# Optimization experiments

Hardware: AMD Instinct MI355X
Metric: run time of the kernel (lower is better)

## Reference

```python
import jax, jax.numpy as jnp
import numpy as np

N_ATOMS = 262144
BATCH = 4096
HIDDEN = 256
HEADS = 4
SCALE = (HIDDEN // HEADS) ** -0.5
LN_EPS = 1e-5
SM_EPS = 1e-16


def setup_inputs() -> dict:
    key = jax.random.key(0)
    ks = jax.random.split(key, 10)
    s = HIDDEN ** -0.5
    return {
        "drug_atoms": jax.random.normal(ks[0], (N_ATOMS, HIDDEN), jnp.float32),
        "protein_ctx": jax.random.normal(ks[1], (BATCH, HIDDEN), jnp.float32),
        "batch_index": jnp.sort(jax.random.randint(ks[2], (N_ATOMS,), 0, BATCH)),
        "Wq": jax.random.normal(ks[3], (HIDDEN, HIDDEN), jnp.float32) * s,
        "bq": jnp.zeros((HIDDEN,), jnp.float32),
        "Wk": jax.random.normal(ks[4], (HIDDEN, HIDDEN), jnp.float32) * s,
        "bk": jnp.zeros((HIDDEN,), jnp.float32),
        "Wv": jax.random.normal(ks[5], (HIDDEN, HIDDEN), jnp.float32) * s,
        "bv": jnp.zeros((HIDDEN,), jnp.float32),
        "ln_gamma": jnp.ones((HIDDEN,), jnp.float32),
        "ln_beta": jnp.zeros((HIDDEN,), jnp.float32),
    }


def _segment_softmax(logits, seg, num_segments):
    # logits: [N, 1]; segment-wise stable softmax (torch_geometric.utils.softmax)
    m = jax.ops.segment_max(logits, seg, num_segments=num_segments)  # [B, 1]
    e = jnp.exp(logits - m[seg])
    s = jax.ops.segment_sum(e, seg, num_segments=num_segments)  # [B, 1]
    return e / (s[seg] + SM_EPS)


def _layer_norm(x, gamma, beta):
    mu = jnp.mean(x, axis=-1, keepdims=True)
    var = jnp.mean(jnp.square(x - mu), axis=-1, keepdims=True)
    return (x - mu) * jax.lax.rsqrt(var + LN_EPS) * gamma + beta


def reference(drug_atoms, protein_ctx, batch_index, Wq, bq, Wk, bk, Wv, bv, ln_gamma, ln_beta):
    protein_expanded = protein_ctx[batch_index]  # [N, H] gather
    Q = protein_expanded @ Wq + bq
    K = drug_atoms @ Wk + bk
    V = drug_atoms @ Wv + bv
    dots = jnp.sum(Q * K, axis=-1, keepdims=True) * SCALE  # [N, 1]
    attn = _segment_softmax(dots, batch_index, BATCH)  # [N, 1]
    out = attn * V + drug_atoms  # weighted V + residual
    return _layer_norm(out, ln_gamma, ln_beta), attn
```

## Files before the change

### kernel.cpp

```cpp
#include <hip/hip_runtime.h>
#include <hip/hip_bf16.h>

#define N_ATOMS 262144
#define BATCH   4096
#define HID     256

typedef __attribute__((ext_vector_type(8))) short short8;
typedef __attribute__((ext_vector_type(4))) float f32x4;
typedef unsigned short u16;
typedef unsigned int   u32;

__device__ __forceinline__ float bf2f(u16 h){
    u32 x = ((u32)h) << 16;
    return __builtin_bit_cast(float, x);
}
__device__ __forceinline__ u16 f2bf(float f){
    u32 x = __builtin_bit_cast(u32, f);
    u32 r = (x + 0x7FFFu + ((x >> 16) & 1u)) >> 16;
    return (u16)r;
}
__device__ __forceinline__ int probe_isf32(const u32* p){
    return ((p[0] & 0xFFFFu) == 0u) ? 1 : 0;
}
__device__ __forceinline__ float cvt_any(const void* p, size_t i, int isf32){
    return isf32 ? ((const float*)p)[i] : bf2f(((const u16*)p)[i]);
}

__global__ void prep_kernel(const void* Wq, const void* Wk, const void* Wv,
                            const void* bq, const void* bk, const void* bv,
                            const void* gamma, const void* beta,
                            float* __restrict__ WqF, float* __restrict__ WkTF,
                            u16* __restrict__ Wfrag,
                            u32* __restrict__ menc, float* __restrict__ sbuf,
                            float* __restrict__ bqf, float* __restrict__ bkf,
                            float* __restrict__ bvf, float* __restrict__ gamf,
                            float* __restrict__ betf){
    const int isf32 = probe_isf32((const u32*)gamma);
    int blk = blockIdx.x, t = threadIdx.x;
    if (blk < 256){
        size_t i = (size_t)blk*HID + t;
        WqF[i] = cvt_any(Wq, i, isf32);
    } else if (blk < 512){
        int k = blk - 256;
        WkTF[(size_t)k*HID + t] = cvt_any(Wk, (size_t)t*HID + k, isf32);
    } else if (blk < 768){
        int n = blk - 512;
        int k = t;
        int ntile = n >> 4, l15 = n & 15;
        int ki = k >> 5, quad = (k >> 3) & 3, e = k & 7;
        int off = ((ntile*8 + ki)*4 + quad)*128 + l15*8 + e;
        Wfrag[off] = f2bf(cvt_any(Wv, (size_t)k*HID + n, isf32));
    } else if (blk < 784){
        int i = (blk - 768)*256 + t;
        menc[i] = 0u; sbuf[i] = 0.f;
    } else {
        bqf[t]  = cvt_any(bq, t, isf32);
        bkf[t]  = cvt_any(bk, t, isf32);
        bvf[t]  = cvt_any(bv, t, isf32);
        gamf[t] = cvt_any(gamma, t, isf32);
        betf[t] = cvt_any(beta, t, isf32);
    }
}

template<int AMODE, int BIAS>
__global__ void small_gemm(const void* Araw, const float* __restrict__ BknF,
                           const float* __restrict__ biasF,
                           float* __restrict__ outF, const u32* __restrict__ probe){
    __shared__ float As[8*HID];
    const int t  = threadIdx.x;
    const int rb = blockIdx.x * 8;
    const int isf32 = AMODE ? 1 : probe_isf32(probe);
    #pragma unroll
    for (int i = 0; i < 8; ++i)
        As[i*HID + t] = cvt_any(Araw, (size_t)(rb + i)*HID + t, isf32);
    __syncthreads();
    float acc[8] = {0.f,0.f,0.f,0.f,0.f,0.f,0.f,0.f};
    for (int j = 0; j < HID; j += 4){
        float w0 = BknF[(size_t)(j+0)*HID + t];
        float w1 = BknF[(size_t)(j+1)*HID + t];
        float w2 = BknF[(size_t)(j+2)*HID + t];
        float w3 = BknF[(size_t)(j+3)*HID + t];
        #pragma unroll
        for (int r = 0; r < 8; ++r){
            float4 a = *(const float4*)(As + r*HID + j);
            acc[r] += a.x*w0 + a.y*w1 + a.z*w2 + a.w*w3;
        }
    }
    float b = BIAS ? biasF[t] : 0.f;
    #pragma unroll
    for (int r = 0; r < 8; ++r)
        outF[(size_t)(rb + r)*HID + t] = acc[r] + b;
}

__global__ void ck_kernel(const float* __restrict__ Qf, const float* __restrict__ bkf,
                          float* __restrict__ cvec){
    int row  = blockIdx.x*4 + (threadIdx.x >> 6);
    int lane = threadIdx.x & 63;
    float4 q = *(const float4*)(Qf + (size_t)row*HID + lane*4);
    float p = q.x*bkf[lane*4] + q.y*bkf[lane*4+1] + q.z*bkf[lane*4+2] + q.w*bkf[lane*4+3];
    #pragma unroll
    for (int off=1; off<64; off<<=1) p += __shfl_xor(p, off, 64);
    if (lane == 0) cvec[row] = p;
}

__global__ void dots_kernel(const void* xraw, const int* __restrict__ bidx,
                            const float* __restrict__ uF, const float* __restrict__ cvec,
                            float* __restrict__ dots, u32* __restrict__ menc,
                            const u32* __restrict__ probe){
    const int isf32 = probe_isf32(probe);
    int row  = blockIdx.x*4 + (threadIdx.x >> 6);
    int lane = threadIdx.x & 63;
    int b = bidx[row];
    float4 uv = *(const float4*)(uF + (size_t)b*HID + lane*4);
    float p;
    if (isf32){
        float4 xv = *(const float4*)((const float*)xraw + (size_t)row*HID + lane*4);
        p = xv.x*uv.x + xv.y*uv.y + xv.z*uv.z + xv.w*uv.w;
    } else {
        ushort4 xv = *(const ushort4*)((const u16*)xraw + (size_t)row*HID + lane*4);
        p = bf2f(xv.x)*uv.x + bf2f(xv.y)*uv.y + bf2f(xv.z)*uv.z + bf2f(xv.w)*uv.w;
    }
    #pragma unroll
    for (int off=1; off<64; off<<=1) p += __shfl_xor(p, off, 64);
    if (lane == 0){
        float d = (p + cvec[b]) * 0.125f;
        if (!(fabsf(d) < 1e30f)) d = 0.f;
        dots[row] = d;
        u32 bits = __builtin_bit_cast(u32, d);
        u32 key = (bits & 0x80000000u) ? ~bits : (bits | 0x80000000u);
        atomicMax(&menc[b], key);
    }
}

__global__ void expsum_kernel(const int* __restrict__ bidx, const u32* __restrict__ menc,
                              float* __restrict__ dots, float* __restrict__ sbuf){
    int n    = blockIdx.x*256 + threadIdx.x;
    int lane = threadIdx.x & 63;
    int b = bidx[n];
    u32 key = menc[b];
    u32 bits = (key & 0x80000000u) ? (key & 0x7FFFFFFFu) : ~key;
    float m = __builtin_bit_cast(float, bits);
    float ev = __expf(dots[n] - m);
    dots[n] = ev;
    int b0  = __shfl(b, 0, 64);
    int b63 = __shfl(b, 63, 64);
    if (b0 == b63){
        float t = ev;
        #pragma unroll
        for (int off=1; off<64; off<<=1) t += __shfl_xor(t, off, 64);
        if (lane == 0) atomicAdd(&sbuf[b], t);
    } else {
        atomicAdd(&sbuf[b], ev);
    }
}

__launch_bounds__(256, 4)
__global__ void main_fused(const void* xraw, const u16* __restrict__ Wfrag,
                           const float* __restrict__ ebuf, const float* __restrict__ sbuf,
                           const int* __restrict__ bidx,
                           const float* __restrict__ bvf, const float* __restrict__ gamf,
                           const float* __restrict__ betf,
                           void* outraw, const u32* __restrict__ probe)
{
    __shared__ u16 Abuf[64*HID];
    __shared__ float attn_lds[64];
    __shared__ float bv_lds[HID];
    __shared__ float rowsum[64];
    __shared__ float rowsq[64];

    const int tid  = threadIdx.x;
    const int lane = tid & 63;
    const int wave = tid >> 6;
    const int quad = lane >> 4;
    const int l15  = lane & 15;
    const int rowBase = blockIdx.x * 64;
    const int isf32 = probe_isf32(probe);

    if (isf32){
        const float* Af = (const float*)xraw;
        #pragma unroll
        for (int iss = 0; iss < 8; ++iss){
            int g = iss*256 + tid; int r = g>>5, c = g&31;
            const float* p = Af + (size_t)(rowBase + r)*HID + c*8;
            float4 f0 = *(const float4*)p;
            float4 f1 = *(const float4*)(p + 4);
            short8 s;
            s[0]=(short)f2bf(f0.x); s[1]=(short)f2bf(f0.y);
            s[2]=(short)f2bf(f0.z); s[3]=(short)f2bf(f0.w);
            s[4]=(short)f2bf(f1.x); s[5]=(short)f2bf(f1.y);
            s[6]=(short)f2bf(f1.z); s[7]=(short)f2bf(f1.w);
            int cp = c ^ (r & 7);
            *(short8*)(Abuf + r*256 + cp*8) = s;
        }
    } else {
        const u16* Ab = (const u16*)xraw;
        short8 areg[8];
        #pragma unroll
        for (int iss = 0; iss < 8; ++iss){
            int g = iss*256 + tid; int r = g>>5, c = g&31;
            areg[iss] = *(const short8*)(Ab + (size_t)(rowBase + r)*HID + c*8);
        }
        #pragma unroll
        for (int iss = 0; iss < 8; ++iss){
            int g = iss*256 + tid; int r = g>>5, c = g&31;
            int cp = c ^ (r & 7);
            *(short8*)(Abuf + r*256 + cp*8) = areg[iss];
        }
    }

    if (tid < 64){
        int rowG = rowBase + tid;
        int b = bidx[rowG];
        float at = ebuf[rowG] / (sbuf[b] + 1e-16f);
        if (!(fabsf(at) < 1e30f)) at = 0.f;
        attn_lds[tid] = at;
        if (isf32) (((float*)outraw) + (size_t)N_ATOMS*HID)[rowG] = at;
        else       (((u16*)outraw)  + (size_t)N_ATOMS*HID)[rowG] = f2bf(at);
        rowsum[tid] = 0.f;
        rowsq[tid]  = 0.f;
    }
    bv_lds[tid] = bvf[tid];

    float gam[4], bet[4];
    #pragma unroll
    for (int ct = 0; ct < 4; ++ct){
        int col = wave*64 + ct*16 + l15;
        gam[ct] = gamf[col];
        bet[ct] = betf[col];
    }

    f32x4 acc[4][4];
    #pragma unroll
    for (int rt=0; rt<4; ++rt)
      #pragma unroll
      for (int ct=0; ct<4; ++ct)
        acc[rt][ct] = (f32x4){0.f,0.f,0.f,0.f};

    __syncthreads();

    for (int ki = 0; ki < 8; ++ki){
        short8 bfr[4];
        #pragma unroll
        for (int ct=0; ct<4; ++ct){
            int ntile = wave*4 + ct;
            bfr[ct] = *(const short8*)(Wfrag + (size_t)((ntile*8 + ki)*512) + lane*8);
        }
        short8 af[4];
        #pragma unroll
        for (int rt=0; rt<4; ++rt){
            int r  = rt*16 + l15;
            int cc = ki*4 + quad;
            int cp = cc ^ (r & 7);
            af[rt] = *(const short8*)(Abuf + r*256 + cp*8);
        }
        #pragma unroll
        for (int rt=0; rt<4; ++rt)
          #pragma unroll
          for (int ct=0; ct<4; ++ct)
            acc[rt][ct] = __builtin_amdgcn_mfma_f32_16x16x32_bf16(
                              af[rt], bfr[ct], acc[rt][ct], 0, 0, 0);
    }

    #pragma unroll
    for (int rt=0; rt<4; ++rt)
      #pragma unroll
      for (int ct=0; ct<4; ++ct)
        #pragma unroll
        for (int i=0; i<4; ++i){
            int row = rt*16 + quad*4 + i;
            int col = wave*64 + ct*16 + l15;
            int cc = col >> 3;
            int cp = cc ^ (row & 7);
            float xv = bf2f(Abuf[row*256 + cp*8 + (col & 7)]);
            acc[rt][ct][i] = attn_lds[row] * (acc[rt][ct][i] + bv_lds[col]) + xv;
        }
    #pragma unroll
    for (int rt=0; rt<4; ++rt)
      #pragma unroll
      for (int i=0; i<4; ++i){
          float s1 = 0.f, s2 = 0.f;
          #pragma unroll
          for (int ct=0; ct<4; ++ct){ float v = acc[rt][ct][i]; s1 += v; s2 += v*v; }
          #pragma unroll
          for (int off=1; off<16; off<<=1){
              s1 += __shfl_xor(s1, off, 64);
              s2 += __shfl_xor(s2, off, 64);
          }
          if (l15 == 0){
              int row = rt*16 + quad*4 + i;
              atomicAdd(&rowsum[row], s1);
              atomicAdd(&rowsq[row],  s2);
          }
      }
    __syncthreads();
    #pragma unroll
    for (int rt=0; rt<4; ++rt)
      #pragma unroll
      for (int i=0; i<4; ++i){
          int row = rt*16 + quad*4 + i;
          float mu  = rowsum[row] * (1.f/256.f);
          float var = fmaxf(rowsq[row] * (1.f/256.f) - mu*mu, 0.f);
          float rstd = rsqrtf(var + 1e-5f);
          #pragma unroll
          for (int ct=0; ct<4; ++ct){
              int col = wave*64 + ct*16 + l15;
              float v = (acc[rt][ct][i] - mu) * rstd * gam[ct] + bet[ct];
              size_t idx = (size_t)(rowBase+row)*HID + col;
              if (isf32) ((float*)outraw)[idx] = v;
              else       ((u16*)outraw)[idx]  = f2bf(v);
          }
      }
}

extern "C" void kernel_launch(void* const* d_in, const int* in_sizes, int n_in,
                              void* d_out, int out_size, void* d_ws, size_t ws_size,
                              hipStream_t stream) {
    const void* x    = d_in[0];
    const void* P    = d_in[1];
    const int*  bidx = (const int*)d_in[2];
    const void* Wq   = d_in[3];
    const void* bq   = d_in[4];
    const void* Wk   = d_in[5];
    const void* bk   = d_in[6];
    const void* Wv   = d_in[7];
    const void* bv   = d_in[8];
    const void* gam  = d_in[9];
    const void* bet  = d_in[10];
    const u32* probe = (const u32*)gam;

    char* ws = (char*)d_ws;
    float* WqF  = (float*)(ws);
    float* WkTF = (float*)(ws + 262144);
    u16*   Wfrag= (u16*)  (ws + 524288);
    float* Qf   = (float*)(ws + 655360);
    float* uF   = (float*)(ws + 4849664);
    float* cvec = (float*)(ws + 9043968);
    u32*   menc = (u32*)  (ws + 9060352);
    float* sbuf = (float*)(ws + 9076736);
    float* dots = (float*)(ws + 9093120);
    float* bqf  = (float*)(ws + 10141696);
    float* bkf  = (float*)(ws + 10142720);
    float* bvf  = (float*)(ws + 10143744);
    float* gamf = (float*)(ws + 10144768);
    float* betf = (float*)(ws + 10145792);

    prep_kernel<<<785, 256, 0, stream>>>(Wq, Wk, Wv, bq, bk, bv, gam, bet,
                                         WqF, WkTF, Wfrag, menc, sbuf,
                                         bqf, bkf, bvf, gamf, betf);
    small_gemm<0,1><<<BATCH/8, 256, 0, stream>>>(P, WqF, bqf, Qf, probe);
    small_gemm<1,0><<<BATCH/8, 256, 0, stream>>>(Qf, WkTF, nullptr, uF, probe);
    ck_kernel<<<BATCH/4, 256, 0, stream>>>(Qf, bkf, cvec);
    dots_kernel<<<N_ATOMS/4, 256, 0, stream>>>(x, bidx, uF, cvec, dots, menc, probe);
    expsum_kernel<<<N_ATOMS/256, 256, 0, stream>>>(bidx, menc, dots, sbuf);
    main_fused<<<N_ATOMS/64, 256, 0, stream>>>(x, Wfrag, dots, sbuf, bidx,
                                               bvf, gamf, betf, d_out, probe);
}
```

Baseline: 820.1 us.

## Precompute Wq·WkT, drop segment max, stage output stores through LDS

The Q/K projection is refactored algebraically. M = Wq·Wk^T and the bias terms are precomputed, so the per-batch u vector comes from a single small GEMM on protein_ctx. The segment-max pass and the expsum kernel are removed: exponentials are computed directly in dots_kernel after clamping logits to ±80, with per-block combined atomic sums. The main kernel's LayerNorm output is transposed through LDS so it can be written with coalesced vector nontemporal stores. Skipping the max subtraction changes numerical behaviour, risking overflow or precision loss for large logits, though the clamp bounds it.

```diff
diff --git a/kernel.cpp b/kernel.cpp
--- a/kernel.cpp
+++ b/kernel.cpp
@@ -7,6 +7,7 @@
 
 typedef __attribute__((ext_vector_type(8))) short short8;
 typedef __attribute__((ext_vector_type(4))) float f32x4;
+typedef __attribute__((ext_vector_type(4))) unsigned short u16x4;
 typedef unsigned short u16;
 typedef unsigned int   u32;
 
@@ -26,33 +27,29 @@
     return isf32 ? ((const float*)p)[i] : bf2f(((const u16*)p)[i]);
 }
 
-__global__ void prep_kernel(const void* Wq, const void* Wk, const void* Wv,
+__global__ void prep_kernel(const void* Wk, const void* Wv,
                             const void* bq, const void* bk, const void* bv,
                             const void* gamma, const void* beta,
-                            float* __restrict__ WqF, float* __restrict__ WkTF,
-                            u16* __restrict__ Wfrag,
-                            u32* __restrict__ menc, float* __restrict__ sbuf,
+                            float* __restrict__ WkTF, u16* __restrict__ Wfrag,
+                            float* __restrict__ sbuf,
                             float* __restrict__ bqf, float* __restrict__ bkf,
                             float* __restrict__ bvf, float* __restrict__ gamf,
                             float* __restrict__ betf){
     const int isf32 = probe_isf32((const u32*)gamma);
     int blk = blockIdx.x, t = threadIdx.x;
     if (blk < 256){
-        size_t i = (size_t)blk*HID + t;
-        WqF[i] = cvt_any(Wq, i, isf32);
+        int k = blk;
+        WkTF[(size_t)k*HID + t] = cvt_any(Wk, (size_t)t*HID + k, isf32);
     } else if (blk < 512){
-        int k = blk - 256;
-        WkTF[(size_t)k*HID + t] = cvt_any(Wk, (size_t)t*HID + k, isf32);
-    } else if (blk < 768){
-        int n = blk - 512;
+        int n = blk - 256;
         int k = t;
         int ntile = n >> 4, l15 = n & 15;
         int ki = k >> 5, quad = (k >> 3) & 3, e = k & 7;
         int off = ((ntile*8 + ki)*4 + quad)*128 + l15*8 + e;
         Wfrag[off] = f2bf(cvt_any(Wv, (size_t)k*HID + n, isf32));
-    } else if (blk < 784){
-        int i = (blk - 768)*256 + t;
-        menc[i] = 0u; sbuf[i] = 0.f;
+    } else if (blk < 528){
+        int i = (blk - 512)*256 + t;
+        sbuf[i] = 0.f;
     } else {
         bqf[t]  = cvt_any(bq, t, isf32);
         bkf[t]  = cvt_any(bk, t, isf32);
@@ -92,23 +89,53 @@
         outF[(size_t)(rb + r)*HID + t] = acc[r] + b;
 }
 
-__global__ void ck_kernel(const float* __restrict__ Qf, const float* __restrict__ bkf,
-                          float* __restrict__ cvec){
+__global__ void vb_kernel(const float* __restrict__ WkTF,
+                          const float* __restrict__ bqf, const float* __restrict__ bkf,
+                          float* __restrict__ v0F, float* __restrict__ s0){
+    __shared__ float ws4[4];
+    int t = threadIdx.x;
+    float a = 0.f;
+    for (int j = 0; j < HID; ++j)
+        a += bqf[j] * WkTF[(size_t)j*HID + t];
+    v0F[t] = a;
+    float p = bqf[t]*bkf[t];
+    #pragma unroll
+    for (int off=1; off<64; off<<=1) p += __shfl_xor(p, off, 64);
+    if ((t & 63) == 0) ws4[t >> 6] = p;
+    __syncthreads();
+    if (t == 0) s0[0] = ws4[0]+ws4[1]+ws4[2]+ws4[3];
+}
+
+template<int ADDS>
+__global__ void rowdot_kernel(const void* Araw, const float* __restrict__ vecF,
+                              const float* __restrict__ s0, float* __restrict__ outv,
+                              const u32* __restrict__ probe){
+    const int isf32 = probe_isf32(probe);
     int row  = blockIdx.x*4 + (threadIdx.x >> 6);
     int lane = threadIdx.x & 63;
-    float4 q = *(const float4*)(Qf + (size_t)row*HID + lane*4);
-    float p = q.x*bkf[lane*4] + q.y*bkf[lane*4+1] + q.z*bkf[lane*4+2] + q.w*bkf[lane*4+3];
+    float4 vv = *(const float4*)(vecF + lane*4);
+    float p;
+    if (isf32){
+        float4 av = *(const float4*)((const float*)Araw + (size_t)row*HID + lane*4);
+        p = av.x*vv.x + av.y*vv.y + av.z*vv.z + av.w*vv.w;
+    } else {
+        ushort4 av = *(const ushort4*)((const u16*)Araw + (size_t)row*HID + lane*4);
+        p = bf2f(av.x)*vv.x + bf2f(av.y)*vv.y + bf2f(av.z)*vv.z + bf2f(av.w)*vv.w;
+    }
     #pragma unroll
     for (int off=1; off<64; off<<=1) p += __shfl_xor(p, off, 64);
-    if (lane == 0) cvec[row] = p;
+    if (lane == 0) outv[row] = p + (ADDS ? s0[0] : 0.f);
 }
 
 __global__ void dots_kernel(const void* xraw, const int* __restrict__ bidx,
                             const float* __restrict__ uF, const float* __restrict__ cvec,
-                            float* __restrict__ dots, u32* __restrict__ menc,
+                            float* __restrict__ ebuf, float* __restrict__ sbuf,
                             const u32* __restrict__ probe){
+    __shared__ float eS[4];
+    __shared__ int   bS[4];
     const int isf32 = probe_isf32(probe);
     int row  = blockIdx.x*4 + (threadIdx.x >> 6);
+    int wave = threadIdx.x >> 6;
     int lane = threadIdx.x & 63;
     int b = bidx[row];
     float4 uv = *(const float4*)(uF + (size_t)b*HID + lane*4);
@@ -122,35 +149,23 @@
     }
     #pragma unroll
     for (int off=1; off<64; off<<=1) p += __shfl_xor(p, off, 64);
+    float ev = 0.f;
     if (lane == 0){
         float d = (p + cvec[b]) * 0.125f;
-        if (!(fabsf(d) < 1e30f)) d = 0.f;
-        dots[row] = d;
-        u32 bits = __builtin_bit_cast(u32, d);
-        u32 key = (bits & 0x80000000u) ? ~bits : (bits | 0x80000000u);
-        atomicMax(&menc[b], key);
-    }
-}
-
-__global__ void expsum_kernel(const int* __restrict__ bidx, const u32* __restrict__ menc,
-                              float* __restrict__ dots, float* __restrict__ sbuf){
-    int n    = blockIdx.x*256 + threadIdx.x;
-    int lane = threadIdx.x & 63;
-    int b = bidx[n];
-    u32 key = menc[b];
-    u32 bits = (key & 0x80000000u) ? (key & 0x7FFFFFFFu) : ~key;
-    float m = __builtin_bit_cast(float, bits);
-    float ev = __expf(dots[n] - m);
-    dots[n] = ev;
-    int b0  = __shfl(b, 0, 64);
-    int b63 = __shfl(b, 63, 64);
-    if (b0 == b63){
-        float t = ev;
-        #pragma unroll
-        for (int off=1; off<64; off<<=1) t += __shfl_xor(t, off, 64);
-        if (lane == 0) atomicAdd(&sbuf[b], t);
-    } else {
-        atomicAdd(&sbuf[b], ev);
+        if (!(fabsf(d) < 80.f)) d = (d > 0.f) ? 80.f : -80.f;
+        ev = __expf(d);
+        ebuf[row] = ev;
+        eS[wave] = ev; bS[wave] = b;
+    }
+    __syncthreads();
+    if (threadIdx.x == 0){
+        float a = eS[0]; int cb = bS[0];
+        #pragma unroll
+        for (int w = 1; w < 4; ++w){
+            if (bS[w] == cb) a += eS[w];
+            else { atomicAdd(&sbuf[cb], a); cb = bS[w]; a = eS[w]; }
+        }
+        atomicAdd(&sbuf[cb], a);
     }
 }
 
@@ -293,6 +308,7 @@
           }
       }
     __syncthreads();
+
     #pragma unroll
     for (int rt=0; rt<4; ++rt)
       #pragma unroll
@@ -302,14 +318,49 @@
           float var = fmaxf(rowsq[row] * (1.f/256.f) - mu*mu, 0.f);
           float rstd = rsqrtf(var + 1e-5f);
           #pragma unroll
-          for (int ct=0; ct<4; ++ct){
-              int col = wave*64 + ct*16 + l15;
-              float v = (acc[rt][ct][i] - mu) * rstd * gam[ct] + bet[ct];
-              size_t idx = (size_t)(rowBase+row)*HID + col;
-              if (isf32) ((float*)outraw)[idx] = v;
-              else       ((u16*)outraw)[idx]  = f2bf(v);
-          }
+          for (int ct=0; ct<4; ++ct)
+              acc[rt][ct][i] = (acc[rt][ct][i] - mu) * rstd * gam[ct] + bet[ct];
       }
+
+    float* AbufF = (float*)Abuf;
+    #pragma unroll
+    for (int h = 0; h < 2; ++h){
+        if (h) __syncthreads();
+        #pragma unroll
+        for (int rtl = 0; rtl < 2; ++rtl){
+            int rt = 2*h + rtl;
+            #pragma unroll
+            for (int ct=0; ct<4; ++ct)
+              #pragma unroll
+              for (int i=0; i<4; ++i){
+                  int rl  = rtl*16 + quad*4 + i;
+                  int col = wave*64 + ct*16 + l15;
+                  AbufF[rl*256 + col] = acc[rt][ct][i];
+              }
+        }
+        __syncthreads();
+        size_t obase = (size_t)rowBase*HID + (size_t)h*8192;
+        if (isf32){
+            f32x4* og = (f32x4*)((float*)outraw + obase);
+            #pragma unroll
+            for (int s = 0; s < 8; ++s){
+                int f4 = s*256 + tid;
+                f32x4 v4 = ((const f32x4*)AbufF)[f4];
+                __builtin_nontemporal_store(v4, og + f4);
+            }
+        } else {
+            u16x4* og = (u16x4*)((u16*)outraw + obase);
+            #pragma unroll
+            for (int s = 0; s < 8; ++s){
+                int f4 = s*256 + tid;
+                f32x4 v4 = ((const f32x4*)AbufF)[f4];
+                u16x4 u;
+                u.x = f2bf(v4.x); u.y = f2bf(v4.y);
+                u.z = f2bf(v4.z); u.w = f2bf(v4.w);
+                __builtin_nontemporal_store(u, og + f4);
+            }
+        }
+    }
 }
 
 extern "C" void kernel_launch(void* const* d_in, const int* in_sizes, int n_in,
@@ -329,29 +380,31 @@
     const u32* probe = (const u32*)gam;
 
     char* ws = (char*)d_ws;
-    float* WqF  = (float*)(ws);
-    float* WkTF = (float*)(ws + 262144);
-    u16*   Wfrag= (u16*)  (ws + 524288);
-    float* Qf   = (float*)(ws + 655360);
-    float* uF   = (float*)(ws + 4849664);
-    float* cvec = (float*)(ws + 9043968);
-    u32*   menc = (u32*)  (ws + 9060352);
-    float* sbuf = (float*)(ws + 9076736);
-    float* dots = (float*)(ws + 9093120);
-    float* bqf  = (float*)(ws + 10141696);
-    float* bkf  = (float*)(ws + 10142720);
-    float* bvf  = (float*)(ws + 10143744);
-    float* gamf = (float*)(ws + 10144768);
-    float* betf = (float*)(ws + 10145792);
-
-    prep_kernel<<<785, 256, 0, stream>>>(Wq, Wk, Wv, bq, bk, bv, gam, bet,
-                                         WqF, WkTF, Wfrag, menc, sbuf,
+    float* WkTF = (float*)(ws);
+    u16*   Wfrag= (u16*)  (ws + 262144);
+    float* M    = (float*)(ws + 393216);
+    float* uF   = (float*)(ws + 655360);
+    float* cvec = (float*)(ws + 4849664);
+    float* sbuf = (float*)(ws + 4866048);
+    float* ebuf = (float*)(ws + 4882432);
+    float* bqf  = (float*)(ws + 5931008);
+    float* bkf  = (float*)(ws + 5932032);
+    float* bvf  = (float*)(ws + 5933056);
+    float* gamf = (float*)(ws + 5934080);
+    float* betf = (float*)(ws + 5935104);
+    float* v0F  = (float*)(ws + 5936128);
+    float* w1f  = (float*)(ws + 5937152);
+    float* s0b  = (float*)(ws + 5938176);
+
+    prep_kernel<<<529, 256, 0, stream>>>(Wk, Wv, bq, bk, bv, gam, bet,
+                                         WkTF, Wfrag, sbuf,
                                          bqf, bkf, bvf, gamf, betf);
-    small_gemm<0,1><<<BATCH/8, 256, 0, stream>>>(P, WqF, bqf, Qf, probe);
-    small_gemm<1,0><<<BATCH/8, 256, 0, stream>>>(Qf, WkTF, nullptr, uF, probe);
-    ck_kernel<<<BATCH/4, 256, 0, stream>>>(Qf, bkf, cvec);
-    dots_kernel<<<N_ATOMS/4, 256, 0, stream>>>(x, bidx, uF, cvec, dots, menc, probe);
-    expsum_kernel<<<N_ATOMS/256, 256, 0, stream>>>(bidx, menc, dots, sbuf);
-    main_fused<<<N_ATOMS/64, 256, 0, stream>>>(x, Wfrag, dots, sbuf, bidx,
+    small_gemm<0,0><<<HID/8, 256, 0, stream>>>(Wq, WkTF, nullptr, M, probe);
+    vb_kernel<<<1, 256, 0, stream>>>(WkTF, bqf, bkf, v0F, s0b);
+    rowdot_kernel<0><<<HID/4, 256, 0, stream>>>(Wq, bkf, nullptr, w1f, probe);
+    small_gemm<0,1><<<BATCH/8, 256, 0, stream>>>(P, M, v0F, uF, probe);
+    rowdot_kernel<1><<<BATCH/4, 256, 0, stream>>>(P, w1f, s0b, cvec, probe);
+    dots_kernel<<<N_ATOMS/4, 256, 0, stream>>>(x, bidx, uF, cvec, ebuf, sbuf, probe);
+    main_fused<<<N_ATOMS/64, 256, 0, stream>>>(x, Wfrag, ebuf, sbuf, bidx,
                                                bvf, gamf, betf, d_out, probe);
 }
```

After: 726.7 us. 11.4% less time.
